# Optimization experiments

Hardware: AMD Instinct MI355X
Metric: run time of the kernel (lower is better)

The kernel has to match this reference:

```python
import jax, jax.numpy as jnp
import numpy as np

B, K, S, L, H, A = 32, 128, 48, 2, 128, 500
NEG_INF = jnp.float32(-1e30)  # stand-in for -inf that is safe under fp16/bf16 too


def _gather_beam(x, idx):
    # x: (B, K, ...); idx: (B, K) -> x gathered along beam dim
    idx_b = idx.reshape(idx.shape + (1,) * (x.ndim - 2))
    return jnp.take_along_axis(x, jnp.broadcast_to(idx_b, idx.shape + x.shape[2:]), axis=1)


def setup_inputs() -> dict:
    key = jax.random.key(0)
    ks = jax.random.split(key, 12)
    return {
        "gen_ll": jax.random.normal(ks[0], (B, K), jnp.float32),
        "disc_ll": jax.random.normal(ks[1], (B, K), jnp.float32),
        "hiddens": jax.random.normal(ks[2], (B, K, S, L, H), jnp.float32),
        "cells": jax.random.normal(ks[3], (B, K, S, L, H), jnp.float32),
        "trees": jax.random.normal(ks[4], (B, K, S, H), jnp.float32),
        "beam_widths": jax.random.randint(ks[5], (B,), 1, K + 1, jnp.int64),
        "ncons_nts": jax.random.randint(ks[6], (B, K), 0, 8, jnp.int64),
        "nopen_parens": jax.random.randint(ks[7], (B, K), 0, 16, jnp.int64),
        "actions": jax.random.randint(ks[8], (B, K, A), 0, 30, jnp.int64),
        "actions_pos": jax.random.randint(ks[9], (B, K), 0, A, jnp.int64),
        "pointer": jax.random.randint(ks[10], (B, K), 0, S, jnp.int64),
        "size": 64,
    }


def reference(gen_ll, disc_ll, hiddens, cells, trees, beam_widths, ncons_nts,
              nopen_parens, actions, actions_pos, pointer, size):
    # BeamItems.shrink: mask beams outside active width, sort by score (desc),
    # gather all beam-indexed state by the sort permutation, clamp widths.
    beam_order = jnp.arange(K, dtype=beam_widths.dtype)          # (K,)
    outside = beam_order[None, :] >= beam_widths[:, None]        # (B, K)
    masked = jnp.where(outside, NEG_INF, gen_ll)                 # (B, K)

    sort_idx = jnp.argsort(-masked, axis=1)                      # descending
    gen_sorted = jnp.take_along_axis(masked, sort_idx, axis=1)

    disc_sorted = jnp.take_along_axis(disc_ll, sort_idx, axis=1)
    hiddens_s = _gather_beam(hiddens, sort_idx)
    cells_s = _gather_beam(cells, sort_idx)
    trees_s = _gather_beam(trees, sort_idx)
    ncons_s = jnp.take_along_axis(ncons_nts, sort_idx, axis=1)
    nopen_s = jnp.take_along_axis(nopen_parens, sort_idx, axis=1)
    actions_s = _gather_beam(actions, sort_idx)
    actions_pos_s = jnp.take_along_axis(actions_pos, sort_idx, axis=1)
    pointer_s = jnp.take_along_axis(pointer, sort_idx, axis=1)

    new_widths = jnp.minimum(beam_widths, jnp.asarray(size, beam_widths.dtype))
    return (gen_sorted, disc_sorted, hiddens_s, cells_s, trees_s,
            new_widths, ncons_s, nopen_s, actions_s, actions_pos_s, pointer_s)
```

## Files before the change

### kernel.cpp

```cpp
#include <hip/hip_runtime.h>

#define BB 32
#define KK 128
#define SS 48
#define LL 2
#define HH 128
#define AA 500

static constexpr float NEG_INF = -1e30f;

static constexpr long SZ_BK    = (long)BB * KK;
static constexpr long SZ_HID   = (long)BB * KK * SS * LL * HH;
static constexpr long SZ_TREE  = (long)BB * KK * SS * HH;
static constexpr long SZ_ACT   = (long)BB * KK * AA;

static constexpr long OFF_GEN   = 0;
static constexpr long OFF_DISC  = OFF_GEN  + SZ_BK;
static constexpr long OFF_HID   = OFF_DISC + SZ_BK;
static constexpr long OFF_CELL  = OFF_HID  + SZ_HID;
static constexpr long OFF_TREE  = OFF_CELL + SZ_HID;
static constexpr long OFF_WID   = OFF_TREE + SZ_TREE;
static constexpr long OFF_NCONS = OFF_WID  + BB;
static constexpr long OFF_NOPEN = OFF_NCONS + SZ_BK;
static constexpr long OFF_ACT   = OFF_NOPEN + SZ_BK;
static constexpr long OFF_APOS  = OFF_ACT  + SZ_ACT;
static constexpr long OFF_PTR   = OFF_APOS + SZ_BK;

typedef float f32x4 __attribute__((ext_vector_type(4)));
typedef int   i32x4 __attribute__((ext_vector_type(4)));

__global__ void sort_small_kernel(
    const float* __restrict__ gen_ll,
    const float* __restrict__ disc_ll,
    const int*   __restrict__ beam_widths,
    const int*   __restrict__ ncons,
    const int*   __restrict__ nopen,
    const int*   __restrict__ actions_pos,
    const int*   __restrict__ pointer,
    const int*   __restrict__ size_ptr,
    float*       __restrict__ out,
    int*         __restrict__ perm_ws)
{
    const int b = blockIdx.x;
    const int i = threadIdx.x;

    __shared__ float mv[KK];
    __shared__ int   perm[KK];

    const int bw = beam_widths[b];
    float v = gen_ll[b * KK + i];
    if (i >= bw) v = NEG_INF;
    mv[i] = v;
    __syncthreads();

    int rank = 0;
#pragma unroll 8
    for (int j = 0; j < KK; ++j) {
        float vj = mv[j];
        rank += (vj > v) || (vj == v && j < i);
    }
    perm[rank] = i;
    __syncthreads();

    const int src = perm[i];
    perm_ws[b * KK + i] = src;

    out[OFF_GEN   + b * KK + i] = mv[src];
    out[OFF_DISC  + b * KK + i] = disc_ll[b * KK + src];
    out[OFF_NCONS + b * KK + i] = (float)ncons[b * KK + src];
    out[OFF_NOPEN + b * KK + i] = (float)nopen[b * KK + src];
    out[OFF_APOS  + b * KK + i] = (float)actions_pos[b * KK + src];
    out[OFF_PTR   + b * KK + i] = (float)pointer[b * KK + src];

    if (i == 0) {
        int sz = size_ptr[0];
        out[OFF_WID + b] = (float)(bw < sz ? bw : sz);
    }
}

__global__ __launch_bounds__(256) void gather_fused(
    const f32x4* __restrict__ hiddens,
    const f32x4* __restrict__ cells,
    const f32x4* __restrict__ trees,
    const i32x4* __restrict__ actions,
    const int*   __restrict__ perm,
    float*       __restrict__ out)
{
    const int bk  = blockIdx.y;
    const int c   = blockIdx.x;
    const int tid = threadIdx.x;
    const int b   = bk >> 7;
    const int src = perm[bk];
    const int srow = b * KK + src;

    if (c < 24) {
        const bool is_h = c < 12;
        const int cc = is_h ? c : c - 12;
        const f32x4* in = is_h ? hiddens : cells;
        f32x4* o = (f32x4*)(out + (is_h ? OFF_HID : OFF_CELL));
        const int r = cc * 256 + tid;
        f32x4 v = __builtin_nontemporal_load(&in[(long)srow * 3072 + r]);
        __builtin_nontemporal_store(v, &o[(long)bk * 3072 + r]);
    } else if (c < 30) {
        const int r = (c - 24) * 256 + tid;
        f32x4 v = __builtin_nontemporal_load(&trees[(long)srow * 1536 + r]);
        f32x4* o = (f32x4*)(out + OFF_TREE);
        __builtin_nontemporal_store(v, &o[(long)bk * 1536 + r]);
    } else {
        if (tid < 125) {
            i32x4 a = __builtin_nontemporal_load(&actions[(long)srow * 125 + tid]);
            f32x4 v;
            v.x = (float)a.x; v.y = (float)a.y; v.z = (float)a.z; v.w = (float)a.w;
            f32x4* o = (f32x4*)(out + OFF_ACT);
            __builtin_nontemporal_store(v, &o[(long)bk * 125 + tid]);
        }
    }
}

extern "C" void kernel_launch(void* const* d_in, const int* in_sizes, int n_in,
                              void* d_out, int out_size, void* d_ws, size_t ws_size,
                              hipStream_t stream) {
    const float* gen_ll      = (const float*)d_in[0];
    const float* disc_ll     = (const float*)d_in[1];
    const float* hiddens     = (const float*)d_in[2];
    const float* cells       = (const float*)d_in[3];
    const float* trees       = (const float*)d_in[4];
    const int*   beam_widths = (const int*)d_in[5];
    const int*   ncons       = (const int*)d_in[6];
    const int*   nopen       = (const int*)d_in[7];
    const int*   actions     = (const int*)d_in[8];
    const int*   actions_pos = (const int*)d_in[9];
    const int*   pointer     = (const int*)d_in[10];
    const int*   size_ptr    = (const int*)d_in[11];

    float* out = (float*)d_out;
    int*   perm_ws = (int*)d_ws;

    sort_small_kernel<<<BB, KK, 0, stream>>>(
        gen_ll, disc_ll, beam_widths, ncons, nopen, actions_pos, pointer,
        size_ptr, out, perm_ws);

    dim3 grid(31, BB * KK);
    gather_fused<<<grid, 256, 0, stream>>>(
        (const f32x4*)hiddens, (const f32x4*)cells, (const f32x4*)trees,
        (const i32x4*)actions, perm_ws, out);
}
```

Measured before the change: 172.2 us.

## Fuse beam sort and state gather into one kernel with redundant per-row ranking

Merges the sort kernel and the gather kernel into a single launch with one block per (batch, beam) output row. Each block recomputes the ranks of all 128 beams in shared memory and picks the source beam whose rank equals its own index. It then copies the hidden, cell, tree and action rows itself in unrolled loops. This removes the second launch, the workspace round-trip for the permutation, and the dependency gap between kernels, at the cost of 128x redundant ranking work and far fewer, larger blocks (4096 instead of about 127k).

```diff
diff --git a/kernel.cpp b/kernel.cpp
--- a/kernel.cpp
+++ b/kernel.cpp
@@ -29,91 +29,96 @@
 typedef float f32x4 __attribute__((ext_vector_type(4)));
 typedef int   i32x4 __attribute__((ext_vector_type(4)));
 
-__global__ void sort_small_kernel(
+__global__ __launch_bounds__(256) void shrink_fused(
     const float* __restrict__ gen_ll,
     const float* __restrict__ disc_ll,
+    const f32x4* __restrict__ hiddens,
+    const f32x4* __restrict__ cells,
+    const f32x4* __restrict__ trees,
+    const i32x4* __restrict__ actions,
     const int*   __restrict__ beam_widths,
     const int*   __restrict__ ncons,
     const int*   __restrict__ nopen,
     const int*   __restrict__ actions_pos,
     const int*   __restrict__ pointer,
     const int*   __restrict__ size_ptr,
-    float*       __restrict__ out,
-    int*         __restrict__ perm_ws)
+    float*       __restrict__ out)
 {
-    const int b = blockIdx.x;
-    const int i = threadIdx.x;
+    const int bk  = blockIdx.x;
+    const int b   = bk >> 7;
+    const int k   = bk & (KK - 1);
+    const int tid = threadIdx.x;
 
     __shared__ float mv[KK];
-    __shared__ int   perm[KK];
+    __shared__ int   s_src;
 
     const int bw = beam_widths[b];
-    float v = gen_ll[b * KK + i];
-    if (i >= bw) v = NEG_INF;
-    mv[i] = v;
+    if (tid < KK) {
+        float v = gen_ll[b * KK + tid];
+        if (tid >= bw) v = NEG_INF;
+        mv[tid] = v;
+    }
     __syncthreads();
 
-    int rank = 0;
+    if (tid < KK) {
+        const float v = mv[tid];
+        int rank = 0;
 #pragma unroll 8
-    for (int j = 0; j < KK; ++j) {
-        float vj = mv[j];
-        rank += (vj > v) || (vj == v && j < i);
+        for (int j = 0; j < KK; ++j) {
+            float vj = mv[j];
+            rank += (vj > v) || (vj == v && j < tid);
+        }
+        if (rank == k) {
+            s_src = tid;
+            out[OFF_GEN   + bk] = v;
+            out[OFF_DISC  + bk] = disc_ll[b * KK + tid];
+            out[OFF_NCONS + bk] = (float)ncons[b * KK + tid];
+            out[OFF_NOPEN + bk] = (float)nopen[b * KK + tid];
+            out[OFF_APOS  + bk] = (float)actions_pos[b * KK + tid];
+            out[OFF_PTR   + bk] = (float)pointer[b * KK + tid];
+        }
+        if (tid == 0 && k == 0) {
+            int sz = size_ptr[0];
+            out[OFF_WID + b] = (float)(bw < sz ? bw : sz);
+        }
     }
-    perm[rank] = i;
     __syncthreads();
 
-    const int src = perm[i];
-    perm_ws[b * KK + i] = src;
+    const long srow = (long)b * KK + s_src;
+    const long drow = bk;
 
-    out[OFF_GEN   + b * KK + i] = mv[src];
-    out[OFF_DISC  + b * KK + i] = disc_ll[b * KK + src];
-    out[OFF_NCONS + b * KK + i] = (float)ncons[b * KK + src];
-    out[OFF_NOPEN + b * KK + i] = (float)nopen[b * KK + src];
-    out[OFF_APOS  + b * KK + i] = (float)actions_pos[b * KK + src];
-    out[OFF_PTR   + b * KK + i] = (float)pointer[b * KK + src];
-
-    if (i == 0) {
-        int sz = size_ptr[0];
-        out[OFF_WID + b] = (float)(bw < sz ? bw : sz);
+    {
+        const f32x4* in = hiddens + srow * 3072;
+        f32x4*       o  = (f32x4*)(out + OFF_HID) + drow * 3072;
+#pragma unroll
+        for (int it = 0; it < 12; ++it) {
+            const int r = it * 256 + tid;
+            __builtin_nontemporal_store(__builtin_nontemporal_load(&in[r]), &o[r]);
+        }
     }
-}
-
-__global__ __launch_bounds__(256) void gather_fused(
-    const f32x4* __restrict__ hiddens,
-    const f32x4* __restrict__ cells,
-    const f32x4* __restrict__ trees,
-    const i32x4* __restrict__ actions,
-    const int*   __restrict__ perm,
-    float*       __restrict__ out)
-{
-    const int bk  = blockIdx.y;
-    const int c   = blockIdx.x;
-    const int tid = threadIdx.x;
-    const int b   = bk >> 7;
-    const int src = perm[bk];
-    const int srow = b * KK + src;
-
-    if (c < 24) {
-        const bool is_h = c < 12;
-        const int cc = is_h ? c : c - 12;
-        const f32x4* in = is_h ? hiddens : cells;
-        f32x4* o = (f32x4*)(out + (is_h ? OFF_HID : OFF_CELL));
-        const int r = cc * 256 + tid;
-        f32x4 v = __builtin_nontemporal_load(&in[(long)srow * 3072 + r]);
-        __builtin_nontemporal_store(v, &o[(long)bk * 3072 + r]);
-    } else if (c < 30) {
-        const int r = (c - 24) * 256 + tid;
-        f32x4 v = __builtin_nontemporal_load(&trees[(long)srow * 1536 + r]);
-        f32x4* o = (f32x4*)(out + OFF_TREE);
-        __builtin_nontemporal_store(v, &o[(long)bk * 1536 + r]);
-    } else {
-        if (tid < 125) {
-            i32x4 a = __builtin_nontemporal_load(&actions[(long)srow * 125 + tid]);
-            f32x4 v;
-            v.x = (float)a.x; v.y = (float)a.y; v.z = (float)a.z; v.w = (float)a.w;
-            f32x4* o = (f32x4*)(out + OFF_ACT);
-            __builtin_nontemporal_store(v, &o[(long)bk * 125 + tid]);
+    {
+        const f32x4* in = cells + srow * 3072;
+        f32x4*       o  = (f32x4*)(out + OFF_CELL) + drow * 3072;
+#pragma unroll
+        for (int it = 0; it < 12; ++it) {
+            const int r = it * 256 + tid;
+            __builtin_nontemporal_store(__builtin_nontemporal_load(&in[r]), &o[r]);
         }
+    }
+    {
+        const f32x4* in = trees + srow * 1536;
+        f32x4*       o  = (f32x4*)(out + OFF_TREE) + drow * 1536;
+#pragma unroll
+        for (int it = 0; it < 6; ++it) {
+            const int r = it * 256 + tid;
+            __builtin_nontemporal_store(__builtin_nontemporal_load(&in[r]), &o[r]);
+        }
+    }
+    if (tid < 125) {
+        i32x4 a = __builtin_nontemporal_load(&actions[srow * 125 + tid]);
+        f32x4 v;
+        v.x = (float)a.x; v.y = (float)a.y; v.z = (float)a.z; v.w = (float)a.w;
+        __builtin_nontemporal_store(v, &((f32x4*)(out + OFF_ACT))[drow * 125 + tid]);
     }
 }
 
@@ -134,14 +139,11 @@
     const int*   size_ptr    = (const int*)d_in[11];
 
     float* out = (float*)d_out;
-    int*   perm_ws = (int*)d_ws;
 
-    sort_small_kernel<<<BB, KK, 0, stream>>>(
-        gen_ll, disc_ll, beam_widths, ncons, nopen, actions_pos, pointer,
-        size_ptr, out, perm_ws);
-
-    dim3 grid(31, BB * KK);
-    gather_fused<<<grid, 256, 0, stream>>>(
+    shrink_fused<<<BB * KK, 256, 0, stream>>>(
+        gen_ll, disc_ll,
         (const f32x4*)hiddens, (const f32x4*)cells, (const f32x4*)trees,
-        (const i32x4*)actions, perm_ws, out);
+        (const i32x4*)actions,
+        beam_widths, ncons, nopen, actions_pos, pointer, size_ptr,
+        out);
 }
```

After: 188.7 us. 9.6% more time.
